# Optimization experiments

Hardware: AMD Instinct MI355X
Metric: run time of the kernel (lower is better)

## Reference

```python
import jax, jax.numpy as jnp
import numpy as np

N_NODES = 100000
N_EDGES = 1600000
N_GRAPHS = 512


def gcn_conv(x, src, dst, W, b, num_nodes):
    """PyG GCNConv: add self-loops, sym-normalize, aggregate, add bias."""
    xw = x @ W  # [N, out]
    # degree over destination nodes, +1 for the implicit self-loop
    deg = jax.ops.segment_sum(jnp.ones(src.shape[0], xw.dtype), dst,
                              num_segments=num_nodes) + 1.0
    dinv = jax.lax.rsqrt(deg)  # deg >= 1, safe
    norm = dinv[src] * dinv[dst]  # [E]
    agg = jax.ops.segment_sum(xw[src] * norm[:, None], dst,
                              num_segments=num_nodes)
    # self-loop contribution: dinv[i]^2 * xw[i]
    agg = agg + xw * (dinv * dinv)[:, None]
    return agg + b


def global_mean_pool(x, batch, num_graphs):
    sums = jax.ops.segment_sum(x, batch, num_segments=num_graphs)
    cnts = jax.ops.segment_sum(jnp.ones(x.shape[0], x.dtype), batch,
                               num_segments=num_graphs)
    return sums / jnp.maximum(cnts, 1.0)[:, None]


def setup_inputs() -> dict:
    key = jax.random.key(0)
    ks = jax.random.split(key, 9)
    x = jax.random.normal(ks[0], (N_NODES, 3), dtype=jnp.float32)
    edge_index = jax.random.randint(ks[1], (2, N_EDGES), 0, N_NODES, dtype=jnp.int64)
    batch = jnp.sort(jax.random.randint(ks[2], (N_NODES,), 0, N_GRAPHS, dtype=jnp.int64))
    W1 = jax.random.normal(ks[3], (3, 32), dtype=jnp.float32) * 0.5
    b1 = jax.random.normal(ks[4], (32,), dtype=jnp.float32) * 0.1
    W2 = jax.random.normal(ks[5], (32, 32), dtype=jnp.float32) * 0.2
    b2 = jax.random.normal(ks[6], (32,), dtype=jnp.float32) * 0.1
    Wl = jax.random.normal(ks[7], (32, 2), dtype=jnp.float32) * 0.2
    bl = jax.random.normal(ks[8], (2,), dtype=jnp.float32) * 0.1
    return {"x": x, "edge_index": edge_index, "batch": batch,
            "W1": W1, "b1": b1, "W2": W2, "b2": b2, "Wl": Wl, "bl": bl}


def reference(x, edge_index, batch, W1, b1, W2, b2, Wl, bl):
    src, dst = edge_index[0], edge_index[1]
    h = jax.nn.relu(gcn_conv(x, src, dst, W1, b1, N_NODES))
    h = jax.nn.relu(gcn_conv(h, src, dst, W2, b2, N_NODES))
    g = global_mean_pool(h, batch, N_GRAPHS)  # [G, 32]
    return g @ Wl + bl  # [G, 2]
```

## Files before the change

kernel.cpp:

```cpp
#include <hip/hip_runtime.h>
#include <hip/hip_fp16.h>

#define NN 100000
#define NE 1600000
#define NG 512
#define F  32

#define BSH    8
#define BNODES 256
#define NB     ((NN + BNODES - 1) / BNODES)
#define CAP    5120
#define PCHUNK 4096
#define EPT    8
#define NWGP   ((NE + PCHUNK - 1) / PCHUNK)

__global__ void k_partition(const int* __restrict__ src, const int* __restrict__ dst,
                            int* __restrict__ cursor, int* __restrict__ part) {
    __shared__ int   s_cnt[NB];
    __shared__ int   s_lstart[NB];
    __shared__ int   s_base[NB];
    __shared__ int   wsum[8];
    __shared__ int   lsort[PCHUNK];
    __shared__ short lbkt[PCHUNK];
    int tid = threadIdx.x;
    for (int i = tid; i < NB; i += 512) s_cnt[i] = 0;
    __syncthreads();
    int e0 = blockIdx.x * PCHUNK;
    int rem = NE - e0;
    int pk[EPT]; short bk[EPT];
    int m = 0;
    if (rem >= PCHUNK) {
#pragma unroll
        for (int h = 0; h < 2; ++h) {
            int e = e0 + h * 2048 + tid * 4;
            int4 s4 = *(const int4*)(src + e);
            int4 d4 = *(const int4*)(dst + e);
            int ss[4] = {s4.x, s4.y, s4.z, s4.w};
            int dd[4] = {d4.x, d4.y, d4.z, d4.w};
#pragma unroll
            for (int u = 0; u < 4; ++u) {
                pk[m] = (ss[u] << 8) | (dd[u] & (BNODES - 1));
                bk[m] = (short)(dd[u] >> BSH);
                atomicAdd(&s_cnt[bk[m]], 1);
                ++m;
            }
        }
    } else {
#pragma unroll
        for (int k = 0; k < EPT; ++k) {
            int e = e0 + tid + k * 512;
            if (e < NE) {
                int d = dst[e];
                pk[m] = (src[e] << 8) | (d & (BNODES - 1));
                bk[m] = (short)(d >> BSH);
                atomicAdd(&s_cnt[bk[m]], 1);
                ++m;
            }
        }
    }
    __syncthreads();
    int cv = (tid < NB) ? s_cnt[tid] : 0;
    int v = cv;
#pragma unroll
    for (int o = 1; o < 64; o <<= 1) {
        int t = __shfl_up(v, o, 64);
        if ((tid & 63) >= o) v += t;
    }
    if ((tid & 63) == 63) wsum[tid >> 6] = v;
    __syncthreads();
    int add = 0;
    for (int w = 0; w < (tid >> 6); ++w) add += wsum[w];
    int excl = v + add - cv;
    if (tid < NB) {
        s_lstart[tid] = excl;
        if (cv) s_base[tid] = tid * CAP + atomicAdd(&cursor[tid], cv);
        s_cnt[tid] = 0;
    }
    __syncthreads();
    for (int k = 0; k < m; ++k) {
        int b = bk[k];
        int r = s_lstart[b] + atomicAdd(&s_cnt[b], 1);
        lsort[r] = pk[k];
        lbkt[r]  = (short)b;
    }
    __syncthreads();
    int cnt = min(rem, PCHUNK);
    for (int i = tid; i < cnt; i += 512) {
        int b = lbkt[i];
        part[s_base[b] + (i - s_lstart[b])] = lsort[i];
    }
}

__global__ void k_fill2a(const int* __restrict__ part, const int* __restrict__ cursor,
                         const float* __restrict__ x,
                         int* __restrict__ rowpack, float* __restrict__ dinv,
                         float4* __restrict__ xd) {
    __shared__ int hcnt[BNODES];
    __shared__ int wsum[4];
    int b = blockIdx.x, tid = threadIdx.x;
    int node0 = b << BSH;
    int s0 = b * CAP;
    int ec = cursor[b];
    hcnt[tid] = 0;
    __syncthreads();
    int ctail = ec & ~3;
    for (int i = tid * 4; i < ctail; i += 1024) {
        int4 p = *(const int4*)(part + s0 + i);
        atomicAdd(&hcnt[p.x & (BNODES - 1)], 1);
        atomicAdd(&hcnt[p.y & (BNODES - 1)], 1);
        atomicAdd(&hcnt[p.z & (BNODES - 1)], 1);
        atomicAdd(&hcnt[p.w & (BNODES - 1)], 1);
    }
    if (tid < ec - ctail) atomicAdd(&hcnt[part[s0 + ctail + tid] & (BNODES - 1)], 1);
    __syncthreads();
    int c = hcnt[tid];
    int v = c;
#pragma unroll
    for (int o = 1; o < 64; o <<= 1) {
        int t = __shfl_up(v, o, 64);
        if ((tid & 63) >= o) v += t;
    }
    if ((tid & 63) == 63) wsum[tid >> 6] = v;
    __syncthreads();
    int add = 0;
    for (int w = 0; w < (tid >> 6); ++w) add += wsum[w];
    int excl = v + add - c;
    int n = node0 + tid;
    if (n < NN) {
        rowpack[n] = ((s0 + excl) << 10) | c;
        float d = rsqrtf((float)c + 1.0f);
        dinv[n] = d;
        xd[n] = make_float4(d * x[n * 3 + 0], d * x[n * 3 + 1], d * x[n * 3 + 2], d);
    }
}

__global__ void k_fill2b(const int* __restrict__ part, const int* __restrict__ cursor,
                         const int* __restrict__ rowpack, const float4* __restrict__ xd,
                         const float* __restrict__ W1, const float* __restrict__ b1,
                         int* __restrict__ csr, __half2* __restrict__ g1) {
    __shared__ __align__(16) int lcsr[CAP];
    __shared__ int off[BNODES];
    __shared__ float W1s[3 * F];
    __shared__ float b1s[F];
    int b = blockIdx.x, tid = threadIdx.x;
    int node0 = b << BSH;
    int s0 = b * CAP;
    int cnt = cursor[b];
    if (tid < 3 * F) W1s[tid] = W1[tid];
    if (tid < F) b1s[tid] = b1[tid];
    int n = node0 + tid;
    int pack = (n < NN) ? rowpack[n] : (s0 << 10);
    off[tid] = (pack >> 10) - s0;
    __syncthreads();
    int ctail = cnt & ~3;
    for (int i = tid * 4; i < ctail; i += 1024) {
        int4 p = *(const int4*)(part + s0 + i);
        { int pos = atomicAdd(&off[p.x & (BNODES - 1)], 1); lcsr[pos] = p.x >> 8; }
        { int pos = atomicAdd(&off[p.y & (BNODES - 1)], 1); lcsr[pos] = p.y >> 8; }
        { int pos = atomicAdd(&off[p.z & (BNODES - 1)], 1); lcsr[pos] = p.z >> 8; }
        { int pos = atomicAdd(&off[p.w & (BNODES - 1)], 1); lcsr[pos] = p.w >> 8; }
    }
    if (tid < cnt - ctail) {
        int p = part[s0 + ctail + tid];
        int pos = atomicAdd(&off[p & (BNODES - 1)], 1);
        lcsr[pos] = p >> 8;
    }
    __syncthreads();
    for (int i = tid * 4; i < ctail; i += 1024)
        *(int4*)(csr + s0 + i) = *(const int4*)(lcsr + i);
    if (tid < cnt - ctail) csr[s0 + ctail + tid] = lcsr[ctail + tid];
    if (n < NN) {
        int deg = pack & 1023;
        int beg = (pack >> 10) - s0;
        int end = beg + deg;
        float ax = 0.0f, ay = 0.0f, az = 0.0f;
        int e = beg;
        for (; e + 7 < end; e += 8) {
#pragma unroll
            for (int u = 0; u < 8; ++u) {
                float4 v = xd[lcsr[e + u]];
                ax += v.x; ay += v.y; az += v.z;
            }
        }
        for (; e < end; ++e) {
            float4 v = xd[lcsr[e]];
            ax += v.x; ay += v.y; az += v.z;
        }
        float4 sf = xd[n];
        float dn = sf.w;
        float cx = dn * (ax + sf.x), cy = dn * (ay + sf.y), cz = dn * (az + sf.z);
        __half2 tmp[16];
#pragma unroll
        for (int j = 0; j < 16; ++j) {
            int f0 = 2 * j, f1 = 2 * j + 1;
            float v0 = cx * W1s[f0] + cy * W1s[F + f0] + cz * W1s[2 * F + f0] + b1s[f0];
            float v1 = cx * W1s[f1] + cy * W1s[F + f1] + cz * W1s[2 * F + f1] + b1s[f1];
            tmp[j] = __floats2half2_rn(dn * fmaxf(v0, 0.0f), dn * fmaxf(v1, 0.0f));
        }
        uint4* hv = (uint4*)(g1 + (size_t)n * 16);
        const uint4* tv = (const uint4*)tmp;
        hv[0] = tv[0]; hv[1] = tv[1]; hv[2] = tv[2]; hv[3] = tv[3];
    }
}

__global__ void k_gather2p(const int* __restrict__ rowpack, const int* __restrict__ csr,
                           const __half2* __restrict__ g1, const float* __restrict__ dinv,
                           const int* __restrict__ batch,
                           const float* __restrict__ W2, const float* __restrict__ b2,
                           float* __restrict__ gsum) {
    __shared__ __align__(16) float W2s[F * F];
    __shared__ __align__(16) float b2s[F];
    __shared__ float ts[16][F];
    __shared__ float hs[16][F];
    __shared__ int bat[16];
    int tid = threadIdx.x;
    int nb = blockIdx.x * 16;
    ((float4*)W2s)[tid] = ((const float4*)W2)[tid];
    if (tid < F / 4) ((float4*)b2s)[tid] = ((const float4*)b2)[tid];
    if (tid < 16) bat[tid] = batch[nb + tid];
    int nl = tid >> 4, j = tid & 15;
    int n = nb + nl;
    {
        int pack = rowpack[n];
        int beg = pack >> 10, end = beg + (pack & 1023);
        float ax = 0.0f, ay = 0.0f;
        int e = beg;
        for (; e + 7 < end; e += 8) {
            int s0 = csr[e],     s1 = csr[e + 1], s2 = csr[e + 2], s3 = csr[e + 3];
            int s4 = csr[e + 4], s5 = csr[e + 5], s6 = csr[e + 6], s7 = csr[e + 7];
            float2 v0 = __half22float2(g1[s0 * 16 + j]);
            float2 v1 = __half22float2(g1[s1 * 16 + j]);
            float2 v2 = __half22float2(g1[s2 * 16 + j]);
            float2 v3 = __half22float2(g1[s3 * 16 + j]);
            float2 v4 = __half22float2(g1[s4 * 16 + j]);
            float2 v5 = __half22float2(g1[s5 * 16 + j]);
            float2 v6 = __half22float2(g1[s6 * 16 + j]);
            float2 v7 = __half22float2(g1[s7 * 16 + j]);
            ax += ((v0.x + v1.x) + (v2.x + v3.x)) + ((v4.x + v5.x) + (v6.x + v7.x));
            ay += ((v0.y + v1.y) + (v2.y + v3.y)) + ((v4.y + v5.y) + (v6.y + v7.y));
        }
        for (; e + 3 < end; e += 4) {
            int s0 = csr[e], s1 = csr[e + 1], s2 = csr[e + 2], s3 = csr[e + 3];
            float2 v0 = __half22float2(g1[s0 * 16 + j]);
            float2 v1 = __half22float2(g1[s1 * 16 + j]);
            float2 v2 = __half22float2(g1[s2 * 16 + j]);
            float2 v3 = __half22float2(g1[s3 * 16 + j]);
            ax += (v0.x + v1.x) + (v2.x + v3.x);
            ay += (v0.y + v1.y) + (v2.y + v3.y);
        }
        for (; e < end; ++e) {
            float2 v = __half22float2(g1[csr[e] * 16 + j]);
            ax += v.x; ay += v.y;
        }
        float dn = dinv[n];
        float2 sf = __half22float2(g1[n * 16 + j]);
        ts[nl][2 * j]     = dn * (ax + sf.x);
        ts[nl][2 * j + 1] = dn * (ay + sf.y);
    }
    __syncthreads();
    {
        int f = tid & 31;
        int nn0 = tid >> 5;
#pragma unroll
        for (int pass = 0; pass < 2; ++pass) {
            int nn = nn0 + pass * 8;
            float acc = b2s[f];
#pragma unroll
            for (int k = 0; k < F; ++k) acc += ts[nn][k] * W2s[k * F + f];
            hs[nn][f] = fmaxf(acc, 0.0f);
        }
    }
    __syncthreads();
    if (tid < F) {
        int g0 = bat[0], gmax = bat[15];
        for (int g = g0; g <= gmax; ++g) {
            float s = 0.0f;
#pragma unroll
            for (int i = 0; i < 16; ++i) if (bat[i] == g) s += hs[i][tid];
            atomicAdd(&gsum[g * F + tid], s);
        }
    }
}

__global__ void k_head(const float* __restrict__ gsum, const int* __restrict__ batch,
                       const float* __restrict__ Wl, const float* __restrict__ bl,
                       float* __restrict__ out) {
    int g = blockIdx.x * blockDim.x + threadIdx.x;
    if (g >= NG) return;
    int lo = 0, hi = NN;
    while (lo < hi) { int m = (lo + hi) >> 1; if (batch[m] < g) lo = m + 1; else hi = m; }
    int s = lo;
    lo = 0; hi = NN;
    while (lo < hi) { int m = (lo + hi) >> 1; if (batch[m] < g + 1) lo = m + 1; else hi = m; }
    float inv = 1.0f / fmaxf((float)(lo - s), 1.0f);
    float a0 = 0.0f, a1 = 0.0f;
#pragma unroll
    for (int k = 0; k < F; ++k) {
        float m = gsum[g * F + k] * inv;
        a0 += m * Wl[k * 2 + 0];
        a1 += m * Wl[k * 2 + 1];
    }
    out[g * 2 + 0] = a0 + bl[0];
    out[g * 2 + 1] = a1 + bl[1];
}

extern "C" void kernel_launch(void* const* d_in, const int* in_sizes, int n_in,
                              void* d_out, int out_size, void* d_ws, size_t ws_size,
                              hipStream_t stream) {
    const float* x     = (const float*)d_in[0];
    const int*   eidx  = (const int*)d_in[1];
    const int*   batch = (const int*)d_in[2];
    const float* W1    = (const float*)d_in[3];
    const float* b1    = (const float*)d_in[4];
    const float* W2    = (const float*)d_in[5];
    const float* b2    = (const float*)d_in[6];
    const float* Wl    = (const float*)d_in[7];
    const float* bl    = (const float*)d_in[8];
    float*       out   = (float*)d_out;

    const int* src = eidx;
    const int* dst = eidx + NE;

    char* base = (char*)d_ws;
    size_t off = 0;
    auto alloc = [&](size_t bytes) {
        void* p = base + off;
        off = (off + bytes + 127) & ~(size_t)127;
        return p;
    };
    int*     cursor  = (int*)alloc(NB * sizeof(int) + (size_t)NG * F * sizeof(float));
    float*   gsum    = (float*)(cursor + NB);
    int*     rowpack = (int*)alloc(NN * sizeof(int));
    int*     part    = (int*)alloc((size_t)NB * CAP * sizeof(int));
    int*     csr     = (int*)alloc((size_t)NB * CAP * sizeof(int));
    float*   dinv    = (float*)alloc(NN * sizeof(float));
    float4*  xd      = (float4*)alloc(NN * sizeof(float4));
    __half2* g1      = (__half2*)alloc((size_t)NN * 16 * sizeof(__half2));

    const int B = 256;
    const int gG16 = NN / 16;

    hipMemsetAsync(cursor, 0, NB * sizeof(int) + (size_t)NG * F * sizeof(float), stream);

    k_partition<<<NWGP, 512, 0, stream>>>(src, dst, cursor, part);
    k_fill2a   <<<NB,   B,   0, stream>>>(part, cursor, x, rowpack, dinv, xd);
    k_fill2b   <<<NB,   B,   0, stream>>>(part, cursor, rowpack, xd, W1, b1, csr, g1);

    k_gather2p<<<gG16, B, 0, stream>>>(rowpack, csr, g1, dinv, batch, W2, b2, gsum);

    k_head<<<(NG + B - 1) / B, B, 0, stream>>>(gsum, batch, Wl, bl, out);
}
```

Measured before the change: 159.6 us.

## Merge CSR build into degree kernel and split layer-1 gather into warp-cooperative kernel

Fuses the degree-count/scan kernel with the CSR scatter so part is read in one kernel and rowpack is not re-read. The layer-1 aggregation moves out of the build kernel into a new kernel with 8 threads per node: each lane strides over the node's edges, the partial sums are combined with xor shuffles, and each lane writes 4 output features. This replaces the one-thread-per-node serial gather, which suffered load imbalance and low parallelism. The cost is an extra launch and reading csr back from global memory instead of from LDS.

```diff
diff --git a/kernel.cpp b/kernel.cpp
--- a/kernel.cpp
+++ b/kernel.cpp
@@ -91,11 +91,13 @@
     }
 }
 
-__global__ void k_fill2a(const int* __restrict__ part, const int* __restrict__ cursor,
-                         const float* __restrict__ x,
-                         int* __restrict__ rowpack, float* __restrict__ dinv,
-                         float4* __restrict__ xd) {
+__global__ void k_build(const int* __restrict__ part, const int* __restrict__ cursor,
+                        const float* __restrict__ x,
+                        int* __restrict__ rowpack, float* __restrict__ dinv,
+                        float4* __restrict__ xd, int* __restrict__ csr) {
+    __shared__ __align__(16) int lcsr[CAP];
     __shared__ int hcnt[BNODES];
+    __shared__ int off[BNODES];
     __shared__ int wsum[4];
     int b = blockIdx.x, tid = threadIdx.x;
     int node0 = b << BSH;
@@ -132,27 +134,8 @@
         dinv[n] = d;
         xd[n] = make_float4(d * x[n * 3 + 0], d * x[n * 3 + 1], d * x[n * 3 + 2], d);
     }
-}
-
-__global__ void k_fill2b(const int* __restrict__ part, const int* __restrict__ cursor,
-                         const int* __restrict__ rowpack, const float4* __restrict__ xd,
-                         const float* __restrict__ W1, const float* __restrict__ b1,
-                         int* __restrict__ csr, __half2* __restrict__ g1) {
-    __shared__ __align__(16) int lcsr[CAP];
-    __shared__ int off[BNODES];
-    __shared__ float W1s[3 * F];
-    __shared__ float b1s[F];
-    int b = blockIdx.x, tid = threadIdx.x;
-    int node0 = b << BSH;
-    int s0 = b * CAP;
-    int cnt = cursor[b];
-    if (tid < 3 * F) W1s[tid] = W1[tid];
-    if (tid < F) b1s[tid] = b1[tid];
-    int n = node0 + tid;
-    int pack = (n < NN) ? rowpack[n] : (s0 << 10);
-    off[tid] = (pack >> 10) - s0;
-    __syncthreads();
-    int ctail = cnt & ~3;
+    off[tid] = excl;
+    __syncthreads();
     for (int i = tid * 4; i < ctail; i += 1024) {
         int4 p = *(const int4*)(part + s0 + i);
         { int pos = atomicAdd(&off[p.x & (BNODES - 1)], 1); lcsr[pos] = p.x >> 8; }
@@ -160,7 +143,7 @@
         { int pos = atomicAdd(&off[p.z & (BNODES - 1)], 1); lcsr[pos] = p.z >> 8; }
         { int pos = atomicAdd(&off[p.w & (BNODES - 1)], 1); lcsr[pos] = p.w >> 8; }
     }
-    if (tid < cnt - ctail) {
+    if (tid < ec - ctail) {
         int p = part[s0 + ctail + tid];
         int pos = atomicAdd(&off[p & (BNODES - 1)], 1);
         lcsr[pos] = p >> 8;
@@ -168,39 +151,48 @@
     __syncthreads();
     for (int i = tid * 4; i < ctail; i += 1024)
         *(int4*)(csr + s0 + i) = *(const int4*)(lcsr + i);
-    if (tid < cnt - ctail) csr[s0 + ctail + tid] = lcsr[ctail + tid];
-    if (n < NN) {
-        int deg = pack & 1023;
-        int beg = (pack >> 10) - s0;
-        int end = beg + deg;
-        float ax = 0.0f, ay = 0.0f, az = 0.0f;
-        int e = beg;
-        for (; e + 7 < end; e += 8) {
-#pragma unroll
-            for (int u = 0; u < 8; ++u) {
-                float4 v = xd[lcsr[e + u]];
-                ax += v.x; ay += v.y; az += v.z;
-            }
-        }
-        for (; e < end; ++e) {
-            float4 v = xd[lcsr[e]];
-            ax += v.x; ay += v.y; az += v.z;
-        }
-        float4 sf = xd[n];
-        float dn = sf.w;
-        float cx = dn * (ax + sf.x), cy = dn * (ay + sf.y), cz = dn * (az + sf.z);
-        __half2 tmp[16];
-#pragma unroll
-        for (int j = 0; j < 16; ++j) {
-            int f0 = 2 * j, f1 = 2 * j + 1;
-            float v0 = cx * W1s[f0] + cy * W1s[F + f0] + cz * W1s[2 * F + f0] + b1s[f0];
-            float v1 = cx * W1s[f1] + cy * W1s[F + f1] + cz * W1s[2 * F + f1] + b1s[f1];
-            tmp[j] = __floats2half2_rn(dn * fmaxf(v0, 0.0f), dn * fmaxf(v1, 0.0f));
-        }
-        uint4* hv = (uint4*)(g1 + (size_t)n * 16);
-        const uint4* tv = (const uint4*)tmp;
-        hv[0] = tv[0]; hv[1] = tv[1]; hv[2] = tv[2]; hv[3] = tv[3];
-    }
+    if (tid < ec - ctail) csr[s0 + ctail + tid] = lcsr[ctail + tid];
+}
+
+#define L1NPB 32
+__global__ void k_l1(const int* __restrict__ rowpack, const int* __restrict__ csr,
+                     const float4* __restrict__ xd,
+                     const float* __restrict__ W1, const float* __restrict__ b1,
+                     __half2* __restrict__ g1) {
+    __shared__ float W1s[3 * F];
+    __shared__ float b1s[F];
+    int tid = threadIdx.x;
+    if (tid < 3 * F) W1s[tid] = W1[tid];
+    if (tid < F) b1s[tid] = b1[tid];
+    __syncthreads();
+    int nl = tid >> 3, l8 = tid & 7;
+    int n = blockIdx.x * L1NPB + nl;
+    if (n >= NN) return;
+    int pack = rowpack[n];
+    int beg = pack >> 10, deg = pack & 1023;
+    float ax = 0.0f, ay = 0.0f, az = 0.0f;
+    for (int e = beg + l8; e < beg + deg; e += 8) {
+        float4 v = xd[csr[e]];
+        ax += v.x; ay += v.y; az += v.z;
+    }
+#pragma unroll
+    for (int o = 1; o < 8; o <<= 1) {
+        ax += __shfl_xor(ax, o, 8);
+        ay += __shfl_xor(ay, o, 8);
+        az += __shfl_xor(az, o, 8);
+    }
+    float4 sf = xd[n];
+    float dn = sf.w;
+    float cx = dn * (ax + sf.x), cy = dn * (ay + sf.y), cz = dn * (az + sf.z);
+    __half2 tmp[2];
+#pragma unroll
+    for (int t = 0; t < 2; ++t) {
+        int f0 = l8 * 4 + 2 * t, f1 = f0 + 1;
+        float v0 = cx * W1s[f0] + cy * W1s[F + f0] + cz * W1s[2 * F + f0] + b1s[f0];
+        float v1 = cx * W1s[f1] + cy * W1s[F + f1] + cz * W1s[2 * F + f1] + b1s[f1];
+        tmp[t] = __floats2half2_rn(dn * fmaxf(v0, 0.0f), dn * fmaxf(v1, 0.0f));
+    }
+    *(uint2*)(g1 + (size_t)n * 16 + l8 * 2) = *(const uint2*)tmp;
 }
 
 __global__ void k_gather2p(const int* __restrict__ rowpack, const int* __restrict__ csr,
@@ -338,13 +330,15 @@
     __half2* g1      = (__half2*)alloc((size_t)NN * 16 * sizeof(__half2));
 
     const int B = 256;
+    const int gL1  = (NN + L1NPB - 1) / L1NPB;
     const int gG16 = NN / 16;
 
     hipMemsetAsync(cursor, 0, NB * sizeof(int) + (size_t)NG * F * sizeof(float), stream);
 
     k_partition<<<NWGP, 512, 0, stream>>>(src, dst, cursor, part);
-    k_fill2a   <<<NB,   B,   0, stream>>>(part, cursor, x, rowpack, dinv, xd);
-    k_fill2b   <<<NB,   B,   0, stream>>>(part, cursor, rowpack, xd, W1, b1, csr, g1);
+    k_build    <<<NB,   B,   0, stream>>>(part, cursor, x, rowpack, dinv, xd, csr);
+
+    k_l1<<<gL1, B, 0, stream>>>(rowpack, csr, xd, W1, b1, g1);
 
     k_gather2p<<<gG16, B, 0, stream>>>(rowpack, csr, g1, dinv, batch, W2, b2, gsum);
 
```

Measured after the change: 156.8 us. No clear change (-1.8%).
